# Performance work log

Hardware: AMD Instinct MI355X
Metric: run time of the kernel (lower is better)

Reference implementation:

```python
import jax, jax.numpy as jnp
import numpy as np

GRID = 14  # encoded_image_size

def _grid_edge_index():
    # Exact replica of build_adjacency_matrix().nonzero(): 8-neighbor 14x14 grid.
    edges = []
    for r in range(GRID):
        for c in range(GRID):
            i = r * GRID + c
            for rr in range(max(0, r - 1), min(r + 2, GRID)):
                for cc in range(max(0, c - 1), min(c + 2, GRID)):
                    if rr == r and cc == c:
                        continue
                    edges.append((i, rr * GRID + cc))
    return np.asarray(edges, dtype=np.int64).T  # (2, 1404)


def setup_inputs() -> dict:
    key = jax.random.key(0)
    k1, k2, k3 = jax.random.split(key, 3)
    B, H, W, C, Hid = 128, 14, 14, 2048, 1024
    x = jax.random.normal(k1, (B, H, W, C), dtype=jnp.float32)
    edge_index = jnp.asarray(_grid_edge_index())
    W1 = jax.random.normal(k2, (C, Hid), dtype=jnp.float32) * (1.0 / np.sqrt(C))
    b1 = jnp.zeros((Hid,), jnp.float32)
    W2 = jax.random.normal(k3, (Hid, C), dtype=jnp.float32) * (1.0 / np.sqrt(Hid))
    b2 = jnp.zeros((C,), jnp.float32)
    return {"x": x, "edge_index": edge_index, "W1": W1, "b1": b1, "W2": W2, "b2": b2}


def _gcn_conv(h, W, b, src, dst, dinv):
    # PyG GCNConv: linear transform, symmetric deg-normalized (A+I) aggregation, bias.
    h = h @ W  # [N, out]
    norm = (dinv[src] * dinv[dst])[:, None]
    agg = jax.ops.segment_sum(h[src] * norm, dst, num_segments=h.shape[0])
    agg = agg + h * (dinv * dinv)[:, None]  # self-loop term, norm = 1/deg_i
    return agg + b


def reference(x, edge_index, W1, b1, W2, b2):
    B, H, Wd, C = x.shape
    N = B * H * Wd
    # Faithful to original: permute(0,3,1,2) then reshape(-1, C) (layout-scrambling).
    xf = jnp.transpose(x, (0, 3, 1, 2)).reshape(-1, C)  # [N, C]
    src, dst = edge_index[0], edge_index[1]
    # Degrees over ALL N nodes: self-loop (=1) everywhere + incoming grid edges
    # (only first 196 nodes have grid neighbors; rest are passthrough).
    deg = jnp.ones((N,), xf.dtype).at[dst].add(1.0)
    dinv = jax.lax.rsqrt(deg)
    h = jax.nn.relu(_gcn_conv(xf, W1, b1, src, dst, dinv))
    h = jax.nn.relu(_gcn_conv(h, W2, b2, src, dst, dinv))
    # reshape + permute(0,3,1,2) + permute(0,2,3,1) == identity back to NHWC.
    return h.reshape(B, H, Wd, C)
```

## Files before the change

kernel.cpp:

```cpp
#include <hip/hip_runtime.h>

typedef float  float4_t __attribute__((ext_vector_type(4)));
typedef __bf16 bf16x8   __attribute__((ext_vector_type(8)));
typedef __bf16 bf16x4   __attribute__((ext_vector_type(4)));

#define BM 128
#define BN 128
#define BK 64

#define GLD16(g, l)                                                        \
    __builtin_amdgcn_global_load_lds(                                      \
        (const __attribute__((address_space(1))) void*)(g),                \
        (__attribute__((address_space(3))) void*)(l), 16, 0, 0)

__global__ __launch_bounds__(256)
void transpose_x_kernel(const float* __restrict__ x, __bf16* __restrict__ A1)
{
    __shared__ float tile[64][33];
    const int b  = blockIdx.z;
    const int pt = blockIdx.y * 32;
    const int ct = blockIdx.x * 64;
    const int t  = threadIdx.x;

    const float* xb = x + (size_t)b * 401408;
    const int c  = t & 63;
    const int pr = t >> 6;
#pragma unroll
    for (int pass = 0; pass < 8; ++pass) {
        int pp = pass * 4 + pr;
        int p  = pt + pp;
        if (p < 196) tile[c][pp] = xb[(size_t)p * 2048 + ct + c];
    }
    __syncthreads();

    const int c2 = t >> 2;
    const int po = (t & 3) * 8;
    const int valid = 196 - pt;
    __bf16* ab = A1 + (size_t)b * 401408 + (size_t)(ct + c2) * 196 + pt + po;
    if (po < valid) {
        bf16x4 v0, v1;
#pragma unroll
        for (int i = 0; i < 4; ++i) v0[i] = (__bf16)tile[c2][po + i];
        *(bf16x4*)ab = v0;
        if (po + 8 <= valid) {
#pragma unroll
            for (int i = 0; i < 4; ++i) v1[i] = (__bf16)tile[c2][po + 4 + i];
            *(bf16x4*)(ab + 4) = v1;
        }
    }
}

__global__ void transpose_w_kernel(const float* __restrict__ W, __bf16* __restrict__ Wt,
                                   int K, int N)
{
    __shared__ float tile[32][33];
    const int kt = blockIdx.x * 32, nt = blockIdx.y * 32;
    const int tx = threadIdx.x, ty = threadIdx.y;
#pragma unroll
    for (int rr = 0; rr < 4; ++rr)
        tile[ty + rr * 8][tx] = W[(size_t)(kt + ty + rr * 8) * N + nt + tx];
    __syncthreads();
#pragma unroll
    for (int rr = 0; rr < 4; ++rr)
        Wt[(size_t)(nt + ty + rr * 8) * K + kt + tx] = (__bf16)tile[tx][ty + rr * 8];
}

template<bool OUT_BF16, int NX, int G>
__global__ __launch_bounds__(256)
void gemm_bt_kernel(const __bf16* __restrict__ A,
                    const __bf16* __restrict__ Bt,
                    const float* __restrict__ bias,
                    void* __restrict__ out,
                    float* __restrict__ raw_out,
                    int M, int N, int K)
{
    __shared__ __bf16 sA[BM * BK];
    __shared__ __bf16 sB[BN * BK];

    const int tid  = threadIdx.x;
    const int wid  = tid >> 6;
    const int lane = tid & 63;

    constexpr int NGROUPS = NX / G;
    constexpr int XPG     = 8 / NGROUPS;
    const int l   = blockIdx.x + NX * blockIdx.y;
    const int r8  = l & 7;
    const int t   = l >> 3;
    const int gid = r8 % NGROUPS;
    const int s   = r8 / NGROUPS;
    const int row0 = ((t / G) * XPG + s) * BM;
    const int col0 = (gid * G + (t % G)) * BN;

    const int wave_m = (wid >> 1) * 64;
    const int wave_n = (wid & 1) * 64;

    float4_t acc[4][4];
#pragma unroll
    for (int i = 0; i < 4; ++i)
#pragma unroll
        for (int j = 0; j < 4; ++j)
            acc[i][j] = (float4_t){0.f, 0.f, 0.f, 0.f};

    const int lrow = lane >> 3;
    const int lcol = (lane & 7) * 8;
    const int mrow = lane & 15;
    const int kq   = (lane >> 4) * 8;

    for (int k0 = 0; k0 < K; k0 += BK) {
        const __bf16* Ab = A  + (size_t)row0 * K + k0;
        const __bf16* Bb = Bt + (size_t)col0 * K + k0;
#pragma unroll
        for (int tt = 0; tt < 4; ++tt) {
            int chunk = wid * 4 + tt;
            int rr = chunk * 8 + lrow;
            GLD16(Ab + (size_t)rr * K + lcol, sA + chunk * 512);
            GLD16(Bb + (size_t)rr * K + lcol, sB + chunk * 512);
        }
        __syncthreads();
#pragma unroll
        for (int kk = 0; kk < BK; kk += 32) {
            bf16x8 af[4], bfr[4];
#pragma unroll
            for (int i = 0; i < 4; ++i)
                af[i] = *(const bf16x8*)&sA[(wave_m + i * 16 + mrow) * BK + kk + kq];
#pragma unroll
            for (int j = 0; j < 4; ++j)
                bfr[j] = *(const bf16x8*)&sB[(wave_n + j * 16 + mrow) * BK + kk + kq];
#pragma unroll
            for (int i = 0; i < 4; ++i)
#pragma unroll
                for (int j = 0; j < 4; ++j)
                    acc[i][j] = __builtin_amdgcn_mfma_f32_16x16x32_bf16(
                        af[i], bfr[j], acc[i][j], 0, 0, 0);
        }
        __syncthreads();
    }

    const int crow = (lane >> 4) * 4;
    const int ccol = lane & 15;
    const bool has_raw = row0 < 196;
#pragma unroll
    for (int i = 0; i < 4; ++i) {
#pragma unroll
        for (int j = 0; j < 4; ++j) {
            int gcol = col0 + wave_n + j * 16 + ccol;
            float bv = bias[gcol];
#pragma unroll
            for (int r = 0; r < 4; ++r) {
                int grow = row0 + wave_m + i * 16 + crow + r;
                float v = acc[i][j][r];
                if (has_raw && grow < 196) raw_out[grow * N + gcol] = v;
                float o = fmaxf(v + bv, 0.f);
                if (OUT_BF16) ((__bf16*)out)[(size_t)grow * N + gcol] = (__bf16)o;
                else          ((float*)out)[(size_t)grow * N + gcol] = o;
            }
        }
    }
}

template<typename OutT>
__global__ void fixup_kernel(const float* __restrict__ raw, const float* __restrict__ bias,
                             OutT* __restrict__ out, int N)
{
    const int q = blockIdx.x;
    const int r = q / 14, c = q % 14;
    int nbr[8];
    int cnt = 0;
    for (int rr = (r > 0 ? r - 1 : 0); rr <= (r < 13 ? r + 1 : 13); ++rr)
        for (int cc = (c > 0 ? c - 1 : 0); cc <= (c < 13 ? c + 1 : 13); ++cc)
            if (!(rr == r && cc == c)) nbr[cnt++] = rr * 14 + cc;
    const float dq    = 1.f / sqrtf(1.f + (float)cnt);
    const float wself = 1.f / (1.f + (float)cnt);
    float wn[8];
    for (int t = 0; t < cnt; ++t) {
        int pr = nbr[t] / 14, pc = nbr[t] % 14;
        int pcnt = ((pr < 13 ? pr + 1 : 13) - (pr > 0 ? pr - 1 : 0) + 1) *
                   ((pc < 13 ? pc + 1 : 13) - (pc > 0 ? pc - 1 : 0) + 1) - 1;
        wn[t] = dq / sqrtf(1.f + (float)pcnt);
    }
    const int ch = blockIdx.y * 256 + threadIdx.x;
    float s = raw[q * N + ch] * wself;
    for (int t = 0; t < cnt; ++t) s += raw[nbr[t] * N + ch] * wn[t];
    float o = fmaxf(s + bias[ch], 0.f);
    out[(size_t)q * N + ch] = (OutT)o;
}

extern "C" void kernel_launch(void* const* d_in, const int* in_sizes, int n_in,
                              void* d_out, int out_size, void* d_ws, size_t ws_size,
                              hipStream_t stream)
{
    const float* x  = (const float*)d_in[0];
    const float* W1 = (const float*)d_in[2];
    const float* b1 = (const float*)d_in[3];
    const float* W2 = (const float*)d_in[4];
    const float* b2 = (const float*)d_in[5];

    const int M = 25088, C = 2048, Hid = 1024;

    __bf16* A1 = (__bf16*)d_out;

    char* ws = (char*)d_ws;
    __bf16* A2    = (__bf16*)(ws);
    __bf16* W1t   = (__bf16*)(ws + 51380224);
    __bf16* W2t   = (__bf16*)(ws + 55574528);
    float*  h1raw = (float*)(ws + 59768832);
    float*  h2raw = (float*)(ws + 60571648);

    transpose_x_kernel<<<dim3(32, 7, 128), 256, 0, stream>>>(x, A1);
    transpose_w_kernel<<<dim3(C / 32, Hid / 32), dim3(32, 8), 0, stream>>>(W1, W1t, C, Hid);
    transpose_w_kernel<<<dim3(Hid / 32, C / 32), dim3(32, 8), 0, stream>>>(W2, W2t, Hid, C);

    gemm_bt_kernel<true, 8, 2><<<dim3(Hid / BN, M / BM), 256, 0, stream>>>(
        A1, W1t, b1, (void*)A2, h1raw, M, Hid, C);
    fixup_kernel<__bf16><<<dim3(196, Hid / 256), 256, 0, stream>>>(h1raw, b1, A2, Hid);

    gemm_bt_kernel<false, 16, 4><<<dim3(C / BN, M / BM), 256, 0, stream>>>(
        A2, W2t, b2, d_out, h2raw, M, C, Hid);
    fixup_kernel<float><<<dim3(196, C / 256), 256, 0, stream>>>(h2raw, b2, (float*)d_out, C);
}
```

Baseline: 749.1 us.

## Swizzle GEMM LDS layout and rewrite x transpose for contiguous vector stores

The GEMM now stores each loaded 16-byte chunk at an XOR-swizzled column position (column group XOR row index) and reads fragments back with the same swizzle. This removes LDS bank conflicts on the MFMA operand reads. Separately, the x transpose kernel now has each block handle 32 channels across all 196 positions, using a padded shared tile. It writes the fully contiguous 32*196 output span with aligned 8-wide bf16 stores, replacing the partial 4-wide stores of the old layout. The cost is a larger shared tile in the transpose and some extra index arithmetic.

```diff
diff --git a/kernel.cpp b/kernel.cpp
--- a/kernel.cpp
+++ b/kernel.cpp
@@ -2,7 +2,6 @@
 
 typedef float  float4_t __attribute__((ext_vector_type(4)));
 typedef __bf16 bf16x8   __attribute__((ext_vector_type(8)));
-typedef __bf16 bf16x4   __attribute__((ext_vector_type(4)));
 
 #define BM 128
 #define BN 128
@@ -16,36 +15,37 @@
 __global__ __launch_bounds__(256)
 void transpose_x_kernel(const float* __restrict__ x, __bf16* __restrict__ A1)
 {
-    __shared__ float tile[64][33];
-    const int b  = blockIdx.z;
-    const int pt = blockIdx.y * 32;
-    const int ct = blockIdx.x * 64;
+    __shared__ float sm[32 * 221];
+    const int b  = blockIdx.y;
+    const int c0 = blockIdx.x * 32;
     const int t  = threadIdx.x;
 
     const float* xb = x + (size_t)b * 401408;
-    const int c  = t & 63;
-    const int pr = t >> 6;
-#pragma unroll
-    for (int pass = 0; pass < 8; ++pass) {
-        int pp = pass * 4 + pr;
-        int p  = pt + pp;
-        if (p < 196) tile[c][pp] = xb[(size_t)p * 2048 + ct + c];
+    const int cl = t & 31;
+    const int p0 = t >> 5;
+#pragma unroll
+    for (int k = 0; k < 25; ++k) {
+        int p = p0 + k * 8;
+        if (p < 196)
+            sm[cl * 221 + p + (p >> 3)] = xb[(size_t)p * 2048 + c0 + cl];
     }
     __syncthreads();
 
-    const int c2 = t >> 2;
-    const int po = (t & 3) * 8;
-    const int valid = 196 - pt;
-    __bf16* ab = A1 + (size_t)b * 401408 + (size_t)(ct + c2) * 196 + pt + po;
-    if (po < valid) {
-        bf16x4 v0, v1;
-#pragma unroll
-        for (int i = 0; i < 4; ++i) v0[i] = (__bf16)tile[c2][po + i];
-        *(bf16x4*)ab = v0;
-        if (po + 8 <= valid) {
-#pragma unroll
-            for (int i = 0; i < 4; ++i) v1[i] = (__bf16)tile[c2][po + 4 + i];
-            *(bf16x4*)(ab + 4) = v1;
+    __bf16* ab = A1 + (size_t)b * 401408 + (size_t)c0 * 196;
+#pragma unroll
+    for (int k = 0; k < 4; ++k) {
+        int o8 = k * 256 + t;
+        if (o8 < 784) {
+            int o  = o8 * 8;
+            int cc = o / 196;
+            int pp = o - cc * 196;
+            bf16x8 v;
+#pragma unroll
+            for (int i = 0; i < 8; ++i) {
+                v[i] = (__bf16)sm[cc * 221 + pp + (pp >> 3)];
+                if (++pp == 196) { pp = 0; ++cc; }
+            }
+            *(bf16x8*)(ab + o) = v;
         }
     }
 }
@@ -102,7 +102,7 @@
             acc[i][j] = (float4_t){0.f, 0.f, 0.f, 0.f};
 
     const int lrow = lane >> 3;
-    const int lcol = (lane & 7) * 8;
+    const int lcol = ((lane & 7) ^ lrow) * 8;
     const int mrow = lane & 15;
     const int kq   = (lane >> 4) * 8;
 
@@ -120,12 +120,17 @@
 #pragma unroll
         for (int kk = 0; kk < BK; kk += 32) {
             bf16x8 af[4], bfr[4];
-#pragma unroll
-            for (int i = 0; i < 4; ++i)
-                af[i] = *(const bf16x8*)&sA[(wave_m + i * 16 + mrow) * BK + kk + kq];
-#pragma unroll
-            for (int j = 0; j < 4; ++j)
-                bfr[j] = *(const bf16x8*)&sB[(wave_n + j * 16 + mrow) * BK + kk + kq];
+            const int g0 = (kk + kq) >> 3;
+#pragma unroll
+            for (int i = 0; i < 4; ++i) {
+                int row = wave_m + i * 16 + mrow;
+                af[i] = *(const bf16x8*)&sA[row * BK + ((g0 ^ (row & 7)) << 3)];
+            }
+#pragma unroll
+            for (int j = 0; j < 4; ++j) {
+                int row = wave_n + j * 16 + mrow;
+                bfr[j] = *(const bf16x8*)&sB[row * BK + ((g0 ^ (row & 7)) << 3)];
+            }
 #pragma unroll
             for (int i = 0; i < 4; ++i)
 #pragma unroll
@@ -206,7 +211,7 @@
     float*  h1raw = (float*)(ws + 59768832);
     float*  h2raw = (float*)(ws + 60571648);
 
-    transpose_x_kernel<<<dim3(32, 7, 128), 256, 0, stream>>>(x, A1);
+    transpose_x_kernel<<<dim3(64, 128), 256, 0, stream>>>(x, A1);
     transpose_w_kernel<<<dim3(C / 32, Hid / 32), dim3(32, 8), 0, stream>>>(W1, W1t, C, Hid);
     transpose_w_kernel<<<dim3(Hid / 32, C / 32), dim3(32, 8), 0, stream>>>(W2, W2t, Hid, C);
 
```

After: 693.1 us. -7.5%, faster.
